# Kernel optimization log

Hardware: AMD Instinct MI355X
Metric: run time of the kernel (lower is better)

## Reference

```python
import jax, jax.numpy as jnp
import numpy as np

NUM_HEADS = 16
NUM_KV_HEADS = 4
HEAD_DIM = 128
MIN_VALUE = -1e9  # fp32 branch of the torch code


def _rotate_half_interleaved(x):
    # stack([-x[...,1::2], x[...,::2]], -1).reshape_as(x)
    x_even = x[..., ::2]
    x_odd = x[..., 1::2]
    return jnp.stack([-x_odd, x_even], axis=-1).reshape(x.shape)


def setup_inputs() -> dict:
    key = jax.random.key(0)
    ks = jax.random.split(key, 7)
    B, S, D = 2, 2048, 2048
    hidden_states = jax.random.normal(ks[0], (B, S, D), dtype=jnp.float32)
    # realistic rope tables
    inv_freq = 1.0 / (100000.0 ** (np.arange(0, HEAD_DIM, 2, dtype=np.float32) / HEAD_DIM))
    t = np.arange(S, dtype=np.float32)
    freqs = np.outer(t, inv_freq)  # (S, HEAD_DIM/2)
    emb = np.repeat(freqs, 2, axis=-1)  # interleaved layout (S, HEAD_DIM)
    cos = jnp.asarray(np.cos(emb), dtype=jnp.float32)
    sin = jnp.asarray(np.sin(emb), dtype=jnp.float32)
    scale = 0.02
    Wq = jax.random.normal(ks[1], (D, D), dtype=jnp.float32) * scale
    Wk = jax.random.normal(ks[2], (D, NUM_KV_HEADS * HEAD_DIM), dtype=jnp.float32) * scale
    Wv = jax.random.normal(ks[3], (D, NUM_KV_HEADS * HEAD_DIM), dtype=jnp.float32) * scale
    Wo = jax.random.normal(ks[4], (D, D), dtype=jnp.float32) * scale
    return {"hidden_states": hidden_states, "cos": cos, "sin": sin,
            "Wq": Wq, "Wk": Wk, "Wv": Wv, "Wo": Wo}


def reference(hidden_states, cos, sin, Wq, Wk, Wv, Wo):
    B, S, D = hidden_states.shape
    H, KV, hd = NUM_HEADS, NUM_KV_HEADS, HEAD_DIM
    q = (hidden_states @ Wq).reshape(B, S, H, hd)
    k = (hidden_states @ Wk).reshape(B, S, KV, hd)
    v = (hidden_states @ Wv).reshape(B, S, KV, hd)

    # RoPE: cos/sin (S, hd) unsqueezed to (S, 1, hd) broadcasting over heads
    c = cos[:, None, :]
    s = sin[:, None, :]
    q = q * c + _rotate_half_interleaved(q) * s
    k = k * c + _rotate_half_interleaved(k) * s

    # repeat_kv (GQA expansion): (B,S,KV,hd) -> (B,S,H,hd)
    rep = H // KV
    k = jnp.repeat(k, rep, axis=2)
    v = jnp.repeat(v, rep, axis=2)

    scores = jnp.einsum('bqhd,bkhd->bhqk', q, k) / jnp.sqrt(jnp.float32(hd))
    causal = jnp.triu(jnp.ones((S, S), dtype=bool), k=1)
    scores = jnp.where(causal[None, None], scores + MIN_VALUE, scores)
    probs = jax.nn.softmax(scores, axis=-1)
    attn = jnp.einsum('bhqk,bkhd->bqhd', probs, v).reshape(B, S, D)
    out = attn @ Wo
    return out
```

## Files before the change

### kernel.cpp

```cpp
#include <hip/hip_runtime.h>

typedef unsigned short u16;
typedef unsigned int u32;
typedef __bf16 bf16x8 __attribute__((ext_vector_type(8)));
typedef float f32x4 __attribute__((ext_vector_type(4)));

__device__ __forceinline__ u16 f2bf(float f) {
  union { float f; u32 u; } v; v.f = f;
  u32 r = v.u + 0x7fffu + ((v.u >> 16) & 1u);
  return (u16)(r >> 16);
}

__device__ __forceinline__ u32 pack2(float a, float b) {
  union { __bf16 h[2]; u32 u; } x;
  x.h[0] = (__bf16)a; x.h[1] = (__bf16)b;
  return x.u;
}

__device__ __forceinline__ bf16x8 ldb128(const u16* p) {
  return *reinterpret_cast<const bf16x8*>(p);
}

__device__ __forceinline__ f32x4 mfma16(bf16x8 a, bf16x8 b, f32x4 c) {
  return __builtin_amdgcn_mfma_f32_16x16x32_bf16(a, b, c, 0, 0, 0);
}

typedef const __attribute__((address_space(1))) u32* gas_p;
typedef __attribute__((address_space(3))) u32* las_p;
__device__ __forceinline__ void gld_lds16(const void* g, void* l) {
  __builtin_amdgcn_global_load_lds((gas_p)(unsigned long long)g,
                                   (las_p)(u32)(unsigned long long)l, 16, 0, 0);
}

__global__ __launch_bounds__(256) void cvt_f32_bf16(const float4* __restrict__ in,
                                                    uint2* __restrict__ out) {
  int i = blockIdx.x * 256 + threadIdx.x;
  float4 v = in[i];
  uint2 r;
  r.x = (u32)f2bf(v.x) | ((u32)f2bf(v.y) << 16);
  r.y = (u32)f2bf(v.z) | ((u32)f2bf(v.w) << 16);
  out[i] = r;
}

__global__ __launch_bounds__(256) void transp_cvt(const float* __restrict__ in,
                                                  u16* __restrict__ out, int R, int C) {
  __shared__ float tile[32][33];
  int n0 = blockIdx.x * 32, k0 = blockIdx.y * 32;
  int tx = threadIdx.x, ty = threadIdx.y;
#pragma unroll
  for (int i = 0; i < 32; i += 8) tile[ty + i][tx] = in[(k0 + ty + i) * C + n0 + tx];
  __syncthreads();
#pragma unroll
  for (int i = 0; i < 32; i += 8) out[(n0 + ty + i) * R + k0 + tx] = f2bf(tile[tx][ty + i]);
}

template<int BN, int WM, int WN, int MODE, int LOADS>
__global__ __launch_bounds__(512) void gemm_pipe(
    const u16* __restrict__ A, const u16* __restrict__ Bt,
    int M, int N, int K,
    const float* __restrict__ cosb, const float* __restrict__ sinb,
    u16* __restrict__ Qb, u16* __restrict__ Kb, u16* __restrict__ Vt,
    float* __restrict__ outf) {
  constexpr int BM = 256;
  constexpr int WTM = BM / WM;
  constexpr int WTN = BN / WN;
  constexpr int MR = WTM / 16;
  constexpr int NR = WTN / 16;
  constexpr int PA = (BM / 8) / 8;
  constexpr int PB = (BN / 8) / 8;

  __shared__ u16 As[2][BM][64];
  __shared__ u16 Bs[2][BN][64];

  const int tid = threadIdx.x;
  const int wv = tid >> 6, lane = tid & 63;
  const int c = lane & 15, g = lane >> 4;
  const int swz = (c & 7) << 4;

  const int nwg = gridDim.x * gridDim.y;
  const int obid = blockIdx.y * gridDim.x + blockIdx.x;
  const int bid = (obid & 7) * (nwg >> 3) + (obid >> 3);
  const int m0 = (bid / gridDim.x) * BM;
  const int n0 = (bid % gridDim.x) * BN;

  const int wm = wv / WN, wn = wv % WN;

  const int lr = lane >> 3;
  const int lc8 = ((lane & 7) ^ lr) * 8;

  f32x4 acc[MR][NR] = {};
  const int NT = K >> 6;

  auto STAGE = [&](int buf, int t) {
    const int k0 = t * 64;
#pragma unroll
    for (int i = 0; i < PA; i++) {
      const int ch = wv * PA + i;
      gld_lds16(A + (long)(m0 + ch * 8 + lr) * K + k0 + lc8, &As[buf][ch * 8][0]);
    }
#pragma unroll
    for (int i = 0; i < PB; i++) {
      const int ch = wv * PB + i;
      gld_lds16(Bt + (long)(n0 + ch * 8 + lr) * K + k0 + lc8, &Bs[buf][ch * 8][0]);
    }
  };

  auto COMPUTE = [&](int buf) {
#pragma unroll
    for (int kk = 0; kk < 2; kk++) {
      bf16x8 af[MR], bfr[NR];
#pragma unroll
      for (int i = 0; i < MR; i++)
        af[i] = ldb128(&As[buf][wm * WTM + i * 16 + c][((kk * 64 + g * 16) ^ swz) >> 1]);
#pragma unroll
      for (int j = 0; j < NR; j++)
        bfr[j] = ldb128(&Bs[buf][wn * WTN + j * 16 + c][((kk * 64 + g * 16) ^ swz) >> 1]);
      __builtin_amdgcn_s_setprio(1);
#pragma unroll
      for (int i = 0; i < MR; i++)
#pragma unroll
        for (int j = 0; j < NR; j++)
          acc[i][j] = mfma16(af[i], bfr[j], acc[i][j]);
      __builtin_amdgcn_s_setprio(0);
    }
  };

  STAGE(0, 0);
  for (int t = 0; t < NT - 1; ++t) {
    STAGE((t + 1) & 1, t + 1);
    asm volatile("s_waitcnt vmcnt(%0)" :: "i"(LOADS) : "memory");
    __builtin_amdgcn_s_barrier();
    __builtin_amdgcn_sched_barrier(0);
    COMPUTE(t & 1);
    __builtin_amdgcn_sched_barrier(0);
    asm volatile("" ::: "memory");
    __builtin_amdgcn_s_barrier();
  }
  asm volatile("s_waitcnt vmcnt(0)" ::: "memory");
  __builtin_amdgcn_s_barrier();
  COMPUTE((NT - 1) & 1);

  const float q_scale = 0.12751743f;
#pragma unroll
  for (int i = 0; i < MR; i++) {
#pragma unroll
    for (int j = 0; j < NR; j++) {
      const int ncol = n0 + wn * WTN + j * 16 + c;
      if (MODE == 1) {
#pragma unroll
        for (int r = 0; r < 4; r++) {
          const int m = m0 + wm * WTM + i * 16 + g * 4 + r;
          outf[(long)m * N + ncol] = acc[i][j][r];
        }
        continue;
      }
      if (ncol < 2560) {
#pragma unroll
        for (int r = 0; r < 4; r++) {
          const int m = m0 + wm * WTM + i * 16 + g * 4 + r;
          const int s = m & 2047;
          const int d = ncol & 127;
          float val = acc[i][j][r];
          float ct = cosb[s * 128 + d], st = sinb[s * 128 + d];
          float pr = __shfl_xor(val, 1, 64);
          float rot = (ncol & 1) ? pr : -pr;
          float rp = val * ct + rot * st;
          if (ncol < 2048) Qb[m * 2048 + ncol] = f2bf(rp * q_scale);
          else             Kb[m * 512 + (ncol - 2048)] = f2bf(rp);
        }
      } else {
        const int m_base = m0 + wm * WTM + i * 16 + g * 4;
        const int bb = m_base >> 11;
        const int srow = m_base & 2047;
        uint2 pv;
        pv.x = pack2(acc[i][j][0], acc[i][j][1]);
        pv.y = pack2(acc[i][j][2], acc[i][j][3]);
        *(uint2*)&Vt[(bb * 512 + (ncol - 2560)) * 2048 + srow] = pv;
      }
    }
  }
}

__global__ __launch_bounds__(256, 2) void attn_fwd(
    const u16* __restrict__ Qb, const u16* __restrict__ Kb,
    const u16* __restrict__ Vt, u16* __restrict__ attnb) {
  __shared__ u16 Ks[2][64 * 128];
  __shared__ u16 Vs[2][128 * 64];
  __shared__ u16 Pl[4][2][16 * 64];
  const int tid = threadIdx.x;
  const int wv = tid >> 6, lane = tid & 63;
  const int c = lane & 15, g = lane >> 4;
  const int qt = 15 - (int)blockIdx.x;
  const int h = blockIdx.y, b = blockIdx.z;
  const int kvh = h >> 2;
  const int qbase = qt * 128 + wv * 32;
  const int swz = (c & 7) << 4;

  bf16x8 qf0[4], qf1[4];
  {
    const u16* qp0 = Qb + ((b << 11) + qbase + c) * 2048 + h * 128 + g * 8;
#pragma unroll
    for (int dc = 0; dc < 4; dc++) qf0[dc] = ldb128(qp0 + dc * 32);
    const u16* qp1 = qp0 + 16 * 2048;
#pragma unroll
    for (int dc = 0; dc < 4; dc++) qf1[dc] = ldb128(qp1 + dc * 32);
  }

  f32x4 oacc0[8] = {}, oacc1[8] = {};
  float m0r = -1e30f, l0r = 0.f, m1r = -1e30f, l1r = 0.f;

  const int krow = wv * 16 + g;
  const int vrow = wv * 32 + (lane >> 3);
  const u16* Kg = Kb + kvh * 128;
  const u16* Vg = Vt + (b * 512 + kvh * 128) * 2048;
  const int NKV = 2 * qt + 2;

  auto STAGE = [&](int buf, int t) {
    const int k0 = t * 64;
#pragma unroll
    for (int i = 0; i < 4; i++) {
      const int r = krow + i * 4;
      gld_lds16(Kg + ((long)(b * 2048 + k0 + r)) * 512 + ((c ^ (r & 7)) * 8),
                &Ks[buf][(wv * 4 + i) * 512]);
    }
#pragma unroll
    for (int i = 0; i < 4; i++) {
      const int r = vrow + i * 8;
      gld_lds16(Vg + (long)r * 2048 + k0 + (((lane & 7) ^ (r & 7)) * 8),
                &Vs[buf][(wv * 4 + i) * 512]);
    }
  };

  STAGE(0, 0);
  for (int kt = 0; kt < NKV; kt++) {
    const int buf = kt & 1;
    const int k0 = kt * 64;
    if (kt + 1 < NKV) {
      STAGE(buf ^ 1, kt + 1);
      asm volatile("s_waitcnt vmcnt(8)" ::: "memory");
    } else {
      asm volatile("s_waitcnt vmcnt(0)" ::: "memory");
    }
    __builtin_amdgcn_s_barrier();
    __builtin_amdgcn_sched_barrier(0);

    f32x4 t0[4] = {}, t1[4] = {};
#pragma unroll
    for (int kf = 0; kf < 4; kf++) {
#pragma unroll
      for (int dc = 0; dc < 4; dc++) {
        const bf16x8 kfr =
            ldb128(&Ks[buf][(kf * 16 + c) * 128 + (((dc * 64 + g * 16) ^ swz) >> 1)]);
        t0[kf] = mfma16(kfr, qf0[dc], t0[kf]);
        t1[kf] = mfma16(kfr, qf1[dc], t1[kf]);
      }
    }
    if (kt >= NKV - 2) {
      const int q0 = qbase + c, q1 = q0 + 16;
#pragma unroll
      for (int kf = 0; kf < 4; kf++)
#pragma unroll
        for (int r = 0; r < 4; r++) {
          const int key = k0 + kf * 16 + g * 4 + r;
          if (key > q0) t0[kf][r] = -1e30f;
          if (key > q1) t1[kf][r] = -1e30f;
        }
    }
#pragma unroll
    for (int s = 0; s < 2; s++) {
      f32x4* t = s ? t1 : t0;
      float& mr = s ? m1r : m0r;
      float& lr_ = s ? l1r : l0r;
      f32x4* oa = s ? oacc1 : oacc0;
      float pmax = -1e30f;
#pragma unroll
      for (int kf = 0; kf < 4; kf++)
#pragma unroll
        for (int r = 0; r < 4; r++) pmax = fmaxf(pmax, t[kf][r]);
      pmax = fmaxf(pmax, __shfl_xor(pmax, 16, 64));
      pmax = fmaxf(pmax, __shfl_xor(pmax, 32, 64));
      const float mnew = fmaxf(mr, pmax);
      const float scale = __builtin_amdgcn_exp2f(mr - mnew);
      float psum = 0.f;
#pragma unroll
      for (int kf = 0; kf < 4; kf++) {
        float p0 = __builtin_amdgcn_exp2f(t[kf][0] - mnew);
        float p1 = __builtin_amdgcn_exp2f(t[kf][1] - mnew);
        float p2 = __builtin_amdgcn_exp2f(t[kf][2] - mnew);
        float p3 = __builtin_amdgcn_exp2f(t[kf][3] - mnew);
        psum += (p0 + p1) + (p2 + p3);
        u32* pw = (u32*)&Pl[wv][s][c * 64 + (((kf * 32 + g * 8) ^ swz) >> 1)];
        pw[0] = pack2(p0, p1);
        pw[1] = pack2(p2, p3);
      }
      psum += __shfl_xor(psum, 16, 64);
      psum += __shfl_xor(psum, 32, 64);
      lr_ = lr_ * scale + psum;
      mr = mnew;
#pragma unroll
      for (int df = 0; df < 8; df++) oa[df] *= scale;
    }

    const bf16x8 pa0 = ldb128(&Pl[wv][0][c * 64 + (((g * 16) ^ swz) >> 1)]);
    const bf16x8 pa1 = ldb128(&Pl[wv][0][c * 64 + (((64 + g * 16) ^ swz) >> 1)]);
    const bf16x8 pb0 = ldb128(&Pl[wv][1][c * 64 + (((g * 16) ^ swz) >> 1)]);
    const bf16x8 pb1 = ldb128(&Pl[wv][1][c * 64 + (((64 + g * 16) ^ swz) >> 1)]);
#pragma unroll
    for (int df = 0; df < 8; df++) {
      const int vb = (df * 16 + c) * 64;
      const bf16x8 v0 = ldb128(&Vs[buf][vb + (((g * 16) ^ swz) >> 1)]);
      const bf16x8 v1 = ldb128(&Vs[buf][vb + (((64 + g * 16) ^ swz) >> 1)]);
      oacc0[df] = mfma16(v0, pa0, oacc0[df]);
      oacc0[df] = mfma16(v1, pa1, oacc0[df]);
      oacc1[df] = mfma16(v0, pb0, oacc1[df]);
      oacc1[df] = mfma16(v1, pb1, oacc1[df]);
    }
    __builtin_amdgcn_sched_barrier(0);
    asm volatile("" ::: "memory");
    __builtin_amdgcn_s_barrier();
  }

  const float ri0 = 1.f / l0r, ri1 = 1.f / l1r;
  const long ob0 = ((long)(b << 11) + qbase + c) * 2048 + h * 128 + g * 4;
#pragma unroll
  for (int df = 0; df < 8; df++) {
    uint2 o0, o1;
    o0.x = pack2(oacc0[df][0] * ri0, oacc0[df][1] * ri0);
    o0.y = pack2(oacc0[df][2] * ri0, oacc0[df][3] * ri0);
    o1.x = pack2(oacc1[df][0] * ri1, oacc1[df][1] * ri1);
    o1.y = pack2(oacc1[df][2] * ri1, oacc1[df][3] * ri1);
    *(uint2*)&attnb[ob0 + df * 16] = o0;
    *(uint2*)&attnb[ob0 + 16 * 2048 + df * 16] = o1;
  }
}

extern "C" void kernel_launch(void* const* d_in, const int* in_sizes, int n_in,
                              void* d_out, int out_size, void* d_ws, size_t ws_size,
                              hipStream_t stream) {
  const float* X    = (const float*)d_in[0];
  const float* cosb = (const float*)d_in[1];
  const float* sinb = (const float*)d_in[2];
  const float* Wq   = (const float*)d_in[3];
  const float* Wk   = (const float*)d_in[4];
  const float* Wv   = (const float*)d_in[5];
  const float* Wo   = (const float*)d_in[6];

  char* ws = (char*)d_ws;
  u16* Xb    = (u16*)(ws);
  u16* Wt    = (u16*)(ws + 16777216);
  u16* Wot   = (u16*)(ws + 29360128);
  u16* Qb    = (u16*)(ws + 37748736);
  u16* Kb    = (u16*)(ws + 54525952);
  u16* Vt    = (u16*)(ws + 58720256);
  u16* attnb = Xb;

  cvt_f32_bf16<<<dim3(8192), dim3(256), 0, stream>>>((const float4*)X, (uint2*)Xb);
  transp_cvt<<<dim3(64, 64), dim3(32, 8), 0, stream>>>(Wq, Wt, 2048, 2048);
  transp_cvt<<<dim3(16, 64), dim3(32, 8), 0, stream>>>(Wk, Wt + 2048 * 2048, 2048, 512);
  transp_cvt<<<dim3(16, 64), dim3(32, 8), 0, stream>>>(Wv, Wt + 2560 * 2048, 2048, 512);
  transp_cvt<<<dim3(64, 64), dim3(32, 8), 0, stream>>>(Wo, Wot, 2048, 2048);
  gemm_pipe<192, 2, 4, 0, 7><<<dim3(16, 16), dim3(512), 0, stream>>>(
      Xb, Wt, 4096, 3072, 2048, cosb, sinb, Qb, Kb, Vt, nullptr);
  attn_fwd<<<dim3(16, 16, 2), dim3(256), 0, stream>>>(Qb, Kb, Vt, attnb);
  gemm_pipe<128, 4, 2, 1, 6><<<dim3(16, 16), dim3(512), 0, stream>>>(
      attnb, Wot, 4096, 2048, 2048, nullptr, nullptr, nullptr, nullptr, nullptr,
      (float*)d_out);
}
```

Before: 331.7 us.

## Triple-buffer GEMM pipeline and add lazy softmax rescaling in attention

The GEMM kernel becomes a three-stage LDS ring with 256x128 tiles. Loads for stage t+2 are interleaved between the two k-halves of compute, removing the end-of-iteration barrier. The QKV projection grid changes to 24x16. The attention kernel raises wave priority around its MFMA blocks and only rescales the running max and accumulators when the new max exceeds the old by more than 8 (log2 units). This trades exact max tracking for fewer rescale multiplies and adds larger LDS use per GEMM block.

```diff
diff --git a/kernel.cpp b/kernel.cpp
--- a/kernel.cpp
+++ b/kernel.cpp
@@ -54,23 +54,17 @@
   for (int i = 0; i < 32; i += 8) out[(n0 + ty + i) * R + k0 + tx] = f2bf(tile[tx][ty + i]);
 }
 
-template<int BN, int WM, int WN, int MODE, int LOADS>
-__global__ __launch_bounds__(512) void gemm_pipe(
+template<int MODE>
+__global__ __launch_bounds__(512) void gemm_pipe3(
     const u16* __restrict__ A, const u16* __restrict__ Bt,
     int M, int N, int K,
     const float* __restrict__ cosb, const float* __restrict__ sinb,
     u16* __restrict__ Qb, u16* __restrict__ Kb, u16* __restrict__ Vt,
     float* __restrict__ outf) {
-  constexpr int BM = 256;
-  constexpr int WTM = BM / WM;
-  constexpr int WTN = BN / WN;
-  constexpr int MR = WTM / 16;
-  constexpr int NR = WTN / 16;
-  constexpr int PA = (BM / 8) / 8;
-  constexpr int PB = (BN / 8) / 8;
-
-  __shared__ u16 As[2][BM][64];
-  __shared__ u16 Bs[2][BN][64];
+  constexpr int BM = 256, BN = 128;
+
+  __shared__ u16 As[3][BM][64];
+  __shared__ u16 Bs[3][BN][64];
 
   const int tid = threadIdx.x;
   const int wv = tid >> 6, lane = tid & 63;
@@ -83,73 +77,86 @@
   const int m0 = (bid / gridDim.x) * BM;
   const int n0 = (bid % gridDim.x) * BN;
 
-  const int wm = wv / WN, wn = wv % WN;
+  const int wm = wv >> 1, wn = wv & 1;
 
   const int lr = lane >> 3;
   const int lc8 = ((lane & 7) ^ lr) * 8;
 
-  f32x4 acc[MR][NR] = {};
+  f32x4 acc[4][4] = {};
   const int NT = K >> 6;
 
-  auto STAGE = [&](int buf, int t) {
-    const int k0 = t * 64;
-#pragma unroll
-    for (int i = 0; i < PA; i++) {
-      const int ch = wv * PA + i;
-      gld_lds16(A + (long)(m0 + ch * 8 + lr) * K + k0 + lc8, &As[buf][ch * 8][0]);
-    }
-#pragma unroll
-    for (int i = 0; i < PB; i++) {
-      const int ch = wv * PB + i;
-      gld_lds16(Bt + (long)(n0 + ch * 8 + lr) * K + k0 + lc8, &Bs[buf][ch * 8][0]);
-    }
+  auto STAGE_A = [&](int buf, int t, int i) {
+    const int ch = wv * 4 + i;
+    gld_lds16(A + (long)(m0 + ch * 8 + lr) * K + t * 64 + lc8, &As[buf][ch * 8][0]);
   };
-
-  auto COMPUTE = [&](int buf) {
-#pragma unroll
-    for (int kk = 0; kk < 2; kk++) {
-      bf16x8 af[MR], bfr[NR];
-#pragma unroll
-      for (int i = 0; i < MR; i++)
-        af[i] = ldb128(&As[buf][wm * WTM + i * 16 + c][((kk * 64 + g * 16) ^ swz) >> 1]);
-#pragma unroll
-      for (int j = 0; j < NR; j++)
-        bfr[j] = ldb128(&Bs[buf][wn * WTN + j * 16 + c][((kk * 64 + g * 16) ^ swz) >> 1]);
+  auto STAGE_B = [&](int buf, int t, int i) {
+    const int ch = wv * 2 + i;
+    gld_lds16(Bt + (long)(n0 + ch * 8 + lr) * K + t * 64 + lc8, &Bs[buf][ch * 8][0]);
+  };
+  auto STAGE_ALL = [&](int buf, int t) {
+#pragma unroll
+    for (int i = 0; i < 4; i++) STAGE_A(buf, t, i);
+#pragma unroll
+    for (int i = 0; i < 2; i++) STAGE_B(buf, t, i);
+  };
+
+  STAGE_ALL(0, 0);
+  STAGE_ALL(1, 1);
+
+  for (int t = 0; t < NT; ++t) {
+    const int buf = t % 3;
+    if (t < NT - 1) asm volatile("s_waitcnt vmcnt(6)" ::: "memory");
+    else            asm volatile("s_waitcnt vmcnt(0)" ::: "memory");
+    __builtin_amdgcn_s_barrier();
+    __builtin_amdgcn_sched_barrier(0);
+    const bool ds = (t + 2 < NT);
+    const int sbuf = (t + 2) % 3;
+    {
+      bf16x8 af[4], bfr[4];
+#pragma unroll
+      for (int i = 0; i < 4; i++)
+        af[i] = ldb128(&As[buf][wm * 64 + i * 16 + c][((g * 16) ^ swz) >> 1]);
+#pragma unroll
+      for (int j = 0; j < 4; j++)
+        bfr[j] = ldb128(&Bs[buf][wn * 64 + j * 16 + c][((g * 16) ^ swz) >> 1]);
+      if (ds) { STAGE_A(sbuf, t + 2, 0); STAGE_A(sbuf, t + 2, 1); STAGE_B(sbuf, t + 2, 0); }
       __builtin_amdgcn_s_setprio(1);
 #pragma unroll
-      for (int i = 0; i < MR; i++)
-#pragma unroll
-        for (int j = 0; j < NR; j++)
+      for (int i = 0; i < 4; i++)
+#pragma unroll
+        for (int j = 0; j < 4; j++)
           acc[i][j] = mfma16(af[i], bfr[j], acc[i][j]);
       __builtin_amdgcn_s_setprio(0);
     }
-  };
-
-  STAGE(0, 0);
-  for (int t = 0; t < NT - 1; ++t) {
-    STAGE((t + 1) & 1, t + 1);
-    asm volatile("s_waitcnt vmcnt(%0)" :: "i"(LOADS) : "memory");
-    __builtin_amdgcn_s_barrier();
-    __builtin_amdgcn_sched_barrier(0);
-    COMPUTE(t & 1);
-    __builtin_amdgcn_sched_barrier(0);
-    asm volatile("" ::: "memory");
-    __builtin_amdgcn_s_barrier();
-  }
-  asm volatile("s_waitcnt vmcnt(0)" ::: "memory");
-  __builtin_amdgcn_s_barrier();
-  COMPUTE((NT - 1) & 1);
+    {
+      bf16x8 af[4], bfr[4];
+#pragma unroll
+      for (int i = 0; i < 4; i++)
+        af[i] = ldb128(&As[buf][wm * 64 + i * 16 + c][((64 + g * 16) ^ swz) >> 1]);
+#pragma unroll
+      for (int j = 0; j < 4; j++)
+        bfr[j] = ldb128(&Bs[buf][wn * 64 + j * 16 + c][((64 + g * 16) ^ swz) >> 1]);
+      if (ds) { STAGE_A(sbuf, t + 2, 2); STAGE_A(sbuf, t + 2, 3); STAGE_B(sbuf, t + 2, 1); }
+      __builtin_amdgcn_s_setprio(1);
+#pragma unroll
+      for (int i = 0; i < 4; i++)
+#pragma unroll
+        for (int j = 0; j < 4; j++)
+          acc[i][j] = mfma16(af[i], bfr[j], acc[i][j]);
+      __builtin_amdgcn_s_setprio(0);
+    }
+  }
 
   const float q_scale = 0.12751743f;
 #pragma unroll
-  for (int i = 0; i < MR; i++) {
-#pragma unroll
-    for (int j = 0; j < NR; j++) {
-      const int ncol = n0 + wn * WTN + j * 16 + c;
+  for (int i = 0; i < 4; i++) {
+#pragma unroll
+    for (int j = 0; j < 4; j++) {
+      const int ncol = n0 + wn * 64 + j * 16 + c;
       if (MODE == 1) {
 #pragma unroll
         for (int r = 0; r < 4; r++) {
-          const int m = m0 + wm * WTM + i * 16 + g * 4 + r;
+          const int m = m0 + wm * 64 + i * 16 + g * 4 + r;
           outf[(long)m * N + ncol] = acc[i][j][r];
         }
         continue;
@@ -157,7 +164,7 @@
       if (ncol < 2560) {
 #pragma unroll
         for (int r = 0; r < 4; r++) {
-          const int m = m0 + wm * WTM + i * 16 + g * 4 + r;
+          const int m = m0 + wm * 64 + i * 16 + g * 4 + r;
           const int s = m & 2047;
           const int d = ncol & 127;
           float val = acc[i][j][r];
@@ -169,7 +176,7 @@
           else             Kb[m * 512 + (ncol - 2048)] = f2bf(rp);
         }
       } else {
-        const int m_base = m0 + wm * WTM + i * 16 + g * 4;
+        const int m_base = m0 + wm * 64 + i * 16 + g * 4;
         const int bb = m_base >> 11;
         const int srow = m_base & 2047;
         uint2 pv;
@@ -245,6 +252,7 @@
     __builtin_amdgcn_sched_barrier(0);
 
     f32x4 t0[4] = {}, t1[4] = {};
+    __builtin_amdgcn_s_setprio(1);
 #pragma unroll
     for (int kf = 0; kf < 4; kf++) {
 #pragma unroll
@@ -255,6 +263,7 @@
         t1[kf] = mfma16(kfr, qf1[dc], t1[kf]);
       }
     }
+    __builtin_amdgcn_s_setprio(0);
     if (kt >= NKV - 2) {
       const int q0 = qbase + c, q1 = q0 + 16;
 #pragma unroll
@@ -279,15 +288,21 @@
         for (int r = 0; r < 4; r++) pmax = fmaxf(pmax, t[kf][r]);
       pmax = fmaxf(pmax, __shfl_xor(pmax, 16, 64));
       pmax = fmaxf(pmax, __shfl_xor(pmax, 32, 64));
-      const float mnew = fmaxf(mr, pmax);
-      const float scale = __builtin_amdgcn_exp2f(mr - mnew);
+      if (__any(pmax - mr > 8.f)) {
+        const float mnew = fmaxf(mr, pmax);
+        const float scale = __builtin_amdgcn_exp2f(mr - mnew);
+        lr_ *= scale;
+#pragma unroll
+        for (int df = 0; df < 8; df++) oa[df] *= scale;
+        mr = mnew;
+      }
       float psum = 0.f;
 #pragma unroll
       for (int kf = 0; kf < 4; kf++) {
-        float p0 = __builtin_amdgcn_exp2f(t[kf][0] - mnew);
-        float p1 = __builtin_amdgcn_exp2f(t[kf][1] - mnew);
-        float p2 = __builtin_amdgcn_exp2f(t[kf][2] - mnew);
-        float p3 = __builtin_amdgcn_exp2f(t[kf][3] - mnew);
+        float p0 = __builtin_amdgcn_exp2f(t[kf][0] - mr);
+        float p1 = __builtin_amdgcn_exp2f(t[kf][1] - mr);
+        float p2 = __builtin_amdgcn_exp2f(t[kf][2] - mr);
+        float p3 = __builtin_amdgcn_exp2f(t[kf][3] - mr);
         psum += (p0 + p1) + (p2 + p3);
         u32* pw = (u32*)&Pl[wv][s][c * 64 + (((kf * 32 + g * 8) ^ swz) >> 1)];
         pw[0] = pack2(p0, p1);
@@ -295,16 +310,14 @@
       }
       psum += __shfl_xor(psum, 16, 64);
       psum += __shfl_xor(psum, 32, 64);
-      lr_ = lr_ * scale + psum;
-      mr = mnew;
-#pragma unroll
-      for (int df = 0; df < 8; df++) oa[df] *= scale;
+      lr_ += psum;
     }
 
     const bf16x8 pa0 = ldb128(&Pl[wv][0][c * 64 + (((g * 16) ^ swz) >> 1)]);
     const bf16x8 pa1 = ldb128(&Pl[wv][0][c * 64 + (((64 + g * 16) ^ swz) >> 1)]);
     const bf16x8 pb0 = ldb128(&Pl[wv][1][c * 64 + (((g * 16) ^ swz) >> 1)]);
     const bf16x8 pb1 = ldb128(&Pl[wv][1][c * 64 + (((64 + g * 16) ^ swz) >> 1)]);
+    __builtin_amdgcn_s_setprio(1);
 #pragma unroll
     for (int df = 0; df < 8; df++) {
       const int vb = (df * 16 + c) * 64;
@@ -315,6 +328,7 @@
       oacc1[df] = mfma16(v0, pb0, oacc1[df]);
       oacc1[df] = mfma16(v1, pb1, oacc1[df]);
     }
+    __builtin_amdgcn_s_setprio(0);
     __builtin_amdgcn_sched_barrier(0);
     asm volatile("" ::: "memory");
     __builtin_amdgcn_s_barrier();
@@ -359,10 +373,10 @@
   transp_cvt<<<dim3(16, 64), dim3(32, 8), 0, stream>>>(Wk, Wt + 2048 * 2048, 2048, 512);
   transp_cvt<<<dim3(16, 64), dim3(32, 8), 0, stream>>>(Wv, Wt + 2560 * 2048, 2048, 512);
   transp_cvt<<<dim3(64, 64), dim3(32, 8), 0, stream>>>(Wo, Wot, 2048, 2048);
-  gemm_pipe<192, 2, 4, 0, 7><<<dim3(16, 16), dim3(512), 0, stream>>>(
+  gemm_pipe3<0><<<dim3(24, 16), dim3(512), 0, stream>>>(
       Xb, Wt, 4096, 3072, 2048, cosb, sinb, Qb, Kb, Vt, nullptr);
   attn_fwd<<<dim3(16, 16, 2), dim3(256), 0, stream>>>(Qb, Kb, Vt, attnb);
-  gemm_pipe<128, 4, 2, 1, 6><<<dim3(16, 16), dim3(512), 0, stream>>>(
+  gemm_pipe3<1><<<dim3(16, 16), dim3(512), 0, stream>>>(
       attnb, Wot, 4096, 2048, 2048, nullptr, nullptr, nullptr, nullptr, nullptr,
       (float*)d_out);
 }
```

Result: slower. 340.9 us (+2.8%).

## Restructure GEMMs into quarter-tile interleaved pipeline and add lazy softmax rescale

Applied to the files above, without the earlier changes.

Replaces the two-phase GEMM loop with a schedule that splits each K-tile into four quadrant MFMA phases. Each phase interleaves LDS fragment reads, the next tile's global-to-LDS loads and the MFMAs, with finer vmcnt waits. Tile shapes change to 256x256 for QKV (12x16 grid) and 128x256 for the output projection (8x32 grid). In attention it adds setprio around the MFMA blocks and skips the online-softmax rescale unless the running max grows by more than 8 (log2 units). That rescale skip trades a little headroom against overflow for fewer multiplies on the output accumulators.

```diff
diff --git a/kernel.cpp b/kernel.cpp
--- a/kernel.cpp
+++ b/kernel.cpp
@@ -23,6 +23,14 @@
 
 __device__ __forceinline__ f32x4 mfma16(bf16x8 a, bf16x8 b, f32x4 c) {
   return __builtin_amdgcn_mfma_f32_16x16x32_bf16(a, b, c, 0, 0, 0);
+}
+
+template<int N> __device__ __forceinline__ void vwait() {
+  asm volatile("s_waitcnt vmcnt(%0)" :: "i"(N) : "memory");
+}
+__device__ __forceinline__ void lgkm0_fence() {
+  asm volatile("s_waitcnt lgkmcnt(0)" ::: "memory");
+  __builtin_amdgcn_sched_barrier(0);
 }
 
 typedef const __attribute__((address_space(1))) u32* gas_p;
@@ -54,20 +62,18 @@
   for (int i = 0; i < 32; i += 8) out[(n0 + ty + i) * R + k0 + tx] = f2bf(tile[tx][ty + i]);
 }
 
-template<int BN, int WM, int WN, int MODE, int LOADS>
-__global__ __launch_bounds__(512) void gemm_pipe(
+template<int BM, int BN, int MODE, int LA, int LB, int VM>
+__global__ __launch_bounds__(512) void gemm8p(
     const u16* __restrict__ A, const u16* __restrict__ Bt,
     int M, int N, int K,
     const float* __restrict__ cosb, const float* __restrict__ sinb,
     u16* __restrict__ Qb, u16* __restrict__ Kb, u16* __restrict__ Vt,
     float* __restrict__ outf) {
-  constexpr int BM = 256;
-  constexpr int WTM = BM / WM;
-  constexpr int WTN = BN / WN;
-  constexpr int MR = WTM / 16;
-  constexpr int NR = WTN / 16;
-  constexpr int PA = (BM / 8) / 8;
-  constexpr int PB = (BN / 8) / 8;
+  constexpr int WTM = BM / 2, WTN = BN / 4;
+  constexpr int MR = WTM / 16, NR = WTN / 16;
+  constexpr int MH = MR / 2, NH = NR / 2;
+  constexpr int ACH = MH * 2;
+  constexpr int BCH = NH * 2;
 
   __shared__ u16 As[2][BM][64];
   __shared__ u16 Bs[2][BN][64];
@@ -83,7 +89,7 @@
   const int m0 = (bid / gridDim.x) * BM;
   const int n0 = (bid % gridDim.x) * BN;
 
-  const int wm = wv / WN, wn = wv % WN;
+  const int wm = wv >> 2, wn = wv & 3;
 
   const int lr = lane >> 3;
   const int lc8 = ((lane & 7) ^ lr) * 8;
@@ -91,54 +97,88 @@
   f32x4 acc[MR][NR] = {};
   const int NT = K >> 6;
 
-  auto STAGE = [&](int buf, int t) {
-    const int k0 = t * 64;
-#pragma unroll
-    for (int i = 0; i < PA; i++) {
-      const int ch = wv * PA + i;
-      gld_lds16(A + (long)(m0 + ch * 8 + lr) * K + k0 + lc8, &As[buf][ch * 8][0]);
-    }
-#pragma unroll
-    for (int i = 0; i < PB; i++) {
-      const int ch = wv * PB + i;
-      gld_lds16(Bt + (long)(n0 + ch * 8 + lr) * K + k0 + lc8, &Bs[buf][ch * 8][0]);
-    }
-  };
-
-  auto COMPUTE = [&](int buf) {
-#pragma unroll
-    for (int kk = 0; kk < 2; kk++) {
-      bf16x8 af[MR], bfr[NR];
-#pragma unroll
-      for (int i = 0; i < MR; i++)
-        af[i] = ldb128(&As[buf][wm * WTM + i * 16 + c][((kk * 64 + g * 16) ^ swz) >> 1]);
-#pragma unroll
-      for (int j = 0; j < NR; j++)
-        bfr[j] = ldb128(&Bs[buf][wn * WTN + j * 16 + c][((kk * 64 + g * 16) ^ swz) >> 1]);
-      __builtin_amdgcn_s_setprio(1);
-#pragma unroll
-      for (int i = 0; i < MR; i++)
-#pragma unroll
-        for (int j = 0; j < NR; j++)
-          acc[i][j] = mfma16(af[i], bfr[j], acc[i][j]);
-      __builtin_amdgcn_s_setprio(0);
-    }
-  };
-
-  STAGE(0, 0);
-  for (int t = 0; t < NT - 1; ++t) {
-    STAGE((t + 1) & 1, t + 1);
-    asm volatile("s_waitcnt vmcnt(%0)" :: "i"(LOADS) : "memory");
-    __builtin_amdgcn_s_barrier();
-    __builtin_amdgcn_sched_barrier(0);
-    COMPUTE(t & 1);
-    __builtin_amdgcn_sched_barrier(0);
-    asm volatile("" ::: "memory");
-    __builtin_amdgcn_s_barrier();
+  auto STAGE_A = [&](int buf, int t, int hm) {
+#pragma unroll
+    for (int li = 0; li < LA; li++) {
+      const int chg = wv * LA + li;
+      const int rg = chg / ACH, cr = chg % ACH;
+      const int row = rg * WTM + hm * (MH * 16) + cr * 8 + lr;
+      gld_lds16(A + (long)(m0 + row) * K + t * 64 + lc8, &As[buf][row - lr][0]);
+    }
+  };
+  auto STAGE_B = [&](int buf, int t, int hn) {
+#pragma unroll
+    for (int li = 0; li < LB; li++) {
+      const int chg = wv * LB + li;
+      const int rg = chg / BCH, cr = chg % BCH;
+      const int row = rg * WTN + hn * (NH * 16) + cr * 8 + lr;
+      gld_lds16(Bt + (long)(n0 + row) * K + t * 64 + lc8, &Bs[buf][row - lr][0]);
+    }
+  };
+
+  bf16x8 af[MH][2], bfr[NH][2];
+  auto READ_A = [&](int buf, int qm) {
+#pragma unroll
+    for (int i = 0; i < MH; i++)
+#pragma unroll
+      for (int kk = 0; kk < 2; kk++)
+        af[i][kk] = ldb128(&As[buf][wm * WTM + (qm * MH + i) * 16 + c]
+                               [((kk * 64 + g * 16) ^ swz) >> 1]);
+  };
+  auto READ_B = [&](int buf, int qn) {
+#pragma unroll
+    for (int j = 0; j < NH; j++)
+#pragma unroll
+      for (int kk = 0; kk < 2; kk++)
+        bfr[j][kk] = ldb128(&Bs[buf][wn * WTN + (qn * NH + j) * 16 + c]
+                                [((kk * 64 + g * 16) ^ swz) >> 1]);
+  };
+  auto DO_MFMA = [&](int qm, int qn) {
+    __builtin_amdgcn_s_setprio(1);
+#pragma unroll
+    for (int kk = 0; kk < 2; kk++)
+#pragma unroll
+      for (int i = 0; i < MH; i++)
+#pragma unroll
+        for (int j = 0; j < NH; j++)
+          acc[qm * MH + i][qn * NH + j] =
+              mfma16(af[i][kk], bfr[j][kk], acc[qm * MH + i][qn * NH + j]);
+    __builtin_amdgcn_s_setprio(0);
+  };
+
+  STAGE_A(0, 0, 0); STAGE_B(0, 0, 0); STAGE_A(0, 0, 1); STAGE_B(0, 0, 1);
+
+  for (int t = 0; t < NT; ++t) {
+    const int buf = t & 1, nb = buf ^ 1;
+    const bool more = (t + 1 < NT);
+    vwait<VM>();
+    __builtin_amdgcn_s_barrier();
+    __builtin_amdgcn_sched_barrier(0);
+    READ_A(buf, 0); READ_B(buf, 0);
+    if (more) STAGE_A(nb, t + 1, 0);
+    lgkm0_fence();
+    DO_MFMA(0, 0);
+    if (more) vwait<VM>(); else vwait<LB>();
+    __builtin_amdgcn_s_barrier();
+    __builtin_amdgcn_sched_barrier(0);
+    READ_A(buf, 1);
+    if (more) STAGE_B(nb, t + 1, 0);
+    lgkm0_fence();
+    DO_MFMA(1, 0);
+    if (more) vwait<VM>(); else vwait<0>();
+    __builtin_amdgcn_s_barrier();
+    __builtin_amdgcn_sched_barrier(0);
+    READ_B(buf, 1);
+    if (more) STAGE_A(nb, t + 1, 1);
+    lgkm0_fence();
+    DO_MFMA(1, 1);
+    __builtin_amdgcn_s_barrier();
+    __builtin_amdgcn_sched_barrier(0);
+    READ_A(buf, 0);
+    if (more) STAGE_B(nb, t + 1, 1);
+    lgkm0_fence();
+    DO_MFMA(0, 1);
   }
-  asm volatile("s_waitcnt vmcnt(0)" ::: "memory");
-  __builtin_amdgcn_s_barrier();
-  COMPUTE((NT - 1) & 1);
 
   const float q_scale = 0.12751743f;
 #pragma unroll
@@ -245,6 +285,7 @@
     __builtin_amdgcn_sched_barrier(0);
 
     f32x4 t0[4] = {}, t1[4] = {};
+    __builtin_amdgcn_s_setprio(1);
 #pragma unroll
     for (int kf = 0; kf < 4; kf++) {
 #pragma unroll
@@ -255,6 +296,7 @@
         t1[kf] = mfma16(kfr, qf1[dc], t1[kf]);
       }
     }
+    __builtin_amdgcn_s_setprio(0);
     if (kt >= NKV - 2) {
       const int q0 = qbase + c, q1 = q0 + 16;
 #pragma unroll
@@ -279,15 +321,21 @@
         for (int r = 0; r < 4; r++) pmax = fmaxf(pmax, t[kf][r]);
       pmax = fmaxf(pmax, __shfl_xor(pmax, 16, 64));
       pmax = fmaxf(pmax, __shfl_xor(pmax, 32, 64));
-      const float mnew = fmaxf(mr, pmax);
-      const float scale = __builtin_amdgcn_exp2f(mr - mnew);
+      if (__any(pmax - mr > 8.f)) {
+        const float mnew = fmaxf(mr, pmax);
+        const float scale = __builtin_amdgcn_exp2f(mr - mnew);
+        lr_ *= scale;
+#pragma unroll
+        for (int df = 0; df < 8; df++) oa[df] *= scale;
+        mr = mnew;
+      }
       float psum = 0.f;
 #pragma unroll
       for (int kf = 0; kf < 4; kf++) {
-        float p0 = __builtin_amdgcn_exp2f(t[kf][0] - mnew);
-        float p1 = __builtin_amdgcn_exp2f(t[kf][1] - mnew);
-        float p2 = __builtin_amdgcn_exp2f(t[kf][2] - mnew);
-        float p3 = __builtin_amdgcn_exp2f(t[kf][3] - mnew);
+        float p0 = __builtin_amdgcn_exp2f(t[kf][0] - mr);
+        float p1 = __builtin_amdgcn_exp2f(t[kf][1] - mr);
+        float p2 = __builtin_amdgcn_exp2f(t[kf][2] - mr);
+        float p3 = __builtin_amdgcn_exp2f(t[kf][3] - mr);
         psum += (p0 + p1) + (p2 + p3);
         u32* pw = (u32*)&Pl[wv][s][c * 64 + (((kf * 32 + g * 8) ^ swz) >> 1)];
         pw[0] = pack2(p0, p1);
@@ -295,16 +343,14 @@
       }
       psum += __shfl_xor(psum, 16, 64);
       psum += __shfl_xor(psum, 32, 64);
-      lr_ = lr_ * scale + psum;
-      mr = mnew;
-#pragma unroll
-      for (int df = 0; df < 8; df++) oa[df] *= scale;
+      lr_ += psum;
     }
 
     const bf16x8 pa0 = ldb128(&Pl[wv][0][c * 64 + (((g * 16) ^ swz) >> 1)]);
     const bf16x8 pa1 = ldb128(&Pl[wv][0][c * 64 + (((64 + g * 16) ^ swz) >> 1)]);
     const bf16x8 pb0 = ldb128(&Pl[wv][1][c * 64 + (((g * 16) ^ swz) >> 1)]);
     const bf16x8 pb1 = ldb128(&Pl[wv][1][c * 64 + (((64 + g * 16) ^ swz) >> 1)]);
+    __builtin_amdgcn_s_setprio(1);
 #pragma unroll
     for (int df = 0; df < 8; df++) {
       const int vb = (df * 16 + c) * 64;
@@ -315,6 +361,7 @@
       oacc1[df] = mfma16(v0, pb0, oacc1[df]);
       oacc1[df] = mfma16(v1, pb1, oacc1[df]);
     }
+    __builtin_amdgcn_s_setprio(0);
     __builtin_amdgcn_sched_barrier(0);
     asm volatile("" ::: "memory");
     __builtin_amdgcn_s_barrier();
@@ -359,10 +406,10 @@
   transp_cvt<<<dim3(16, 64), dim3(32, 8), 0, stream>>>(Wk, Wt + 2048 * 2048, 2048, 512);
   transp_cvt<<<dim3(16, 64), dim3(32, 8), 0, stream>>>(Wv, Wt + 2560 * 2048, 2048, 512);
   transp_cvt<<<dim3(64, 64), dim3(32, 8), 0, stream>>>(Wo, Wot, 2048, 2048);
-  gemm_pipe<192, 2, 4, 0, 7><<<dim3(16, 16), dim3(512), 0, stream>>>(
+  gemm8p<256, 256, 0, 2, 2, 4><<<dim3(12, 16), dim3(512), 0, stream>>>(
       Xb, Wt, 4096, 3072, 2048, cosb, sinb, Qb, Kb, Vt, nullptr);
   attn_fwd<<<dim3(16, 16, 2), dim3(256), 0, stream>>>(Qb, Kb, Vt, attnb);
-  gemm_pipe<128, 4, 2, 1, 6><<<dim3(16, 16), dim3(512), 0, stream>>>(
+  gemm8p<128, 256, 1, 1, 2, 3><<<dim3(8, 32), dim3(512), 0, stream>>>(
       attnb, Wot, 4096, 2048, 2048, nullptr, nullptr, nullptr, nullptr, nullptr,
       (float*)d_out);
 }
```

Result: slower. 345.2 us (+4.1%).
